# Kernel tuning notes

Measured on AMD Instinct MI355X. Metric: run time of the kernel, lower is better.

Reference implementation:

```python
import jax, jax.numpy as jnp
import numpy as np

V, E, H = 32000, 512, 1024
B, T = 16, 256
EPS = 1e-5

def setup_inputs() -> dict:
    key = jax.random.key(0)
    ks = jax.random.split(key, 20)
    s = lambda *shape: 0.02
    inp = {
        'input': jax.random.randint(ks[0], (B, T), 0, V),
        'embd': jax.random.normal(ks[1], (V, E), jnp.float32) * 0.02,
        # layer 0 GRUCell (input E -> H)
        'Wih0': jax.random.normal(ks[2], (3 * H, E), jnp.float32) * 0.02,
        'Whh0': jax.random.normal(ks[3], (3 * H, H), jnp.float32) * 0.02,
        'bih0': jnp.zeros((3 * H,), jnp.float32),
        'bhh0': jnp.zeros((3 * H,), jnp.float32),
        'ln0_w': jnp.ones((H,), jnp.float32),
        'ln0_b': jnp.zeros((H,), jnp.float32),
        # layer 1 GRUCell (H -> H)
        'Wih1': jax.random.normal(ks[4], (3 * H, H), jnp.float32) * 0.02,
        'Whh1': jax.random.normal(ks[5], (3 * H, H), jnp.float32) * 0.02,
        'bih1': jnp.zeros((3 * H,), jnp.float32),
        'bhh1': jnp.zeros((3 * H,), jnp.float32),
        'ln1_w': jnp.ones((H,), jnp.float32),
        'ln1_b': jnp.zeros((H,), jnp.float32),
        # head: Linear(H,H) -> LeakyReLU -> LayerNorm -> Linear(H,V)
        'W1': jax.random.normal(ks[6], (H, H), jnp.float32) * 0.02,
        'b1': jnp.zeros((H,), jnp.float32),
        'ln2_w': jnp.ones((H,), jnp.float32),
        'ln2_b': jnp.zeros((H,), jnp.float32),
        'W2': jax.random.normal(ks[7], (V, H), jnp.float32) * 0.02,
        'b2': jnp.zeros((V,), jnp.float32),
    }
    return inp

def _layernorm(x, w, b):
    m = jnp.mean(x, axis=-1, keepdims=True)
    v = jnp.var(x, axis=-1, keepdims=True)
    return (x - m) * jax.lax.rsqrt(v + EPS) * w + b

def _gru_cell(x, h, Wih, Whh, bih, bhh):
    gi = x @ Wih.T + bih  # [B, 3H]
    gh = h @ Whh.T + bhh
    ir, iz, inn = jnp.split(gi, 3, axis=-1)
    hr, hz, hn = jnp.split(gh, 3, axis=-1)
    r = jax.nn.sigmoid(ir + hr)
    z = jax.nn.sigmoid(iz + hz)
    n = jnp.tanh(inn + r * hn)
    return (1.0 - z) * n + z * h

def reference(input, embd, Wih0, Whh0, bih0, bhh0, ln0_w, ln0_b,
              Wih1, Whh1, bih1, bhh1, ln1_w, ln1_b,
              W1, b1, ln2_w, ln2_b, W2, b2):
    x = embd[input]                      # [B, T, E]
    xT = jnp.swapaxes(x, 0, 1)           # [T, B, E]
    Bn = input.shape[0]
    h0 = jnp.zeros((Bn, H), x.dtype)
    h1 = jnp.zeros((Bn, H), x.dtype)

    def step(carry, xt):
        h0, h1 = carry
        h0 = _layernorm(_gru_cell(xt, h0, Wih0, Whh0, bih0, bhh0), ln0_w, ln0_b)
        h1 = _layernorm(_gru_cell(h0, h1, Wih1, Whh1, bih1, bhh1), ln1_w, ln1_b)
        a = jax.nn.leaky_relu(h1 @ W1.T + b1, negative_slope=0.01)
        a = _layernorm(a, ln2_w, ln2_b)
        logits = a @ W2.T + b2           # [B, V]
        return (h0, h1), logits

    _, outs = jax.lax.scan(step, (h0, h1), xT)   # [T, B, V]
    return jnp.swapaxes(outs, 0, 1)              # [B, T, V]
```

## Files before the change

kernel.cpp:

```cpp
#include <hip/hip_runtime.h>
#include <stdint.h>
#include <math.h>

#define TT 256
#define VOCAB 32000
#define LN_EPS 1e-5
#define NBLK 256

typedef __attribute__((ext_vector_type(8))) short bf16x8;
typedef __attribute__((ext_vector_type(4))) float f32x4;

__device__ __forceinline__ float bf2f(short s) {
  return __uint_as_float(((uint32_t)(uint16_t)s) << 16);
}
__device__ __forceinline__ short f2bf(float f) {
  uint32_t u = __float_as_uint(f);
  u += 0x7fffu + ((u >> 16) & 1u);
  return (short)(u >> 16);
}
__device__ __forceinline__ f32x4 mfma16(bf16x8 a, bf16x8 b, f32x4 c) {
  return __builtin_amdgcn_mfma_f32_16x16x32_bf16(a, b, c, 0, 0, 0);
}

__device__ __forceinline__ double cload(const double* p) {
  return __hip_atomic_load(p, __ATOMIC_RELAXED, __HIP_MEMORY_SCOPE_AGENT);
}
__device__ __forceinline__ void cstore(double* p, double v) {
  __hip_atomic_store(p, v, __ATOMIC_RELAXED, __HIP_MEMORY_SCOPE_AGENT);
}

__global__ void k_gi0(const int* __restrict__ input, const float* __restrict__ embd,
                      const float* __restrict__ Wih0, const float* __restrict__ bih0,
                      double* __restrict__ gi0) {
  const int t = blockIdx.x >> 4;
  const int cg = blockIdx.x & 15;
  const int tid = threadIdx.x;
  __shared__ float xs[16][512];
  for (int idx = tid; idx < 16 * 512; idx += 256) {
    const int r = idx >> 9, j = idx & 511;
    const int tok = input[r * TT + t];
    xs[r][j] = embd[(size_t)tok * 512 + j];
  }
  __syncthreads();
  const int row = tid >> 4, ct = tid & 15;
  for (int i = 0; i < 12; ++i) {
    const int c = cg * 192 + ct + 16 * i;
    const float4* wp = (const float4*)(Wih0 + (size_t)c * 512);
    const float4* xp = (const float4*)&xs[row][0];
    double acc = 0.0;
#pragma unroll 8
    for (int j4 = 0; j4 < 128; ++j4) {
      const float4 w = wp[j4];
      const float4 x = xp[j4];
      acc = fma((double)x.x, (double)w.x, acc);
      acc = fma((double)x.y, (double)w.y, acc);
      acc = fma((double)x.z, (double)w.z, acc);
      acc = fma((double)x.w, (double)w.w, acc);
    }
    gi0[((size_t)t * 16 + row) * 3072 + c] = acc + (double)bih0[c];
  }
}

struct SP {
  const float *Whh0, *bhh0, *ln0w, *ln0b;
  const float *Wih1, *Whh1, *bih1, *bhh1, *ln1w, *ln1b;
  const double* gi0;
  double *h0ring, *h1ring;
  float* h1hist;
  int* bar;
};

__device__ __forceinline__ void stageC(const double* __restrict__ hrow,
                                       const float* __restrict__ lnw,
                                       const float* __restrict__ lnb,
                                       const int l, double* __restrict__ a,
                                       double& m_out, double& rs_out) {
  double s = 0.0, q = 0.0;
#pragma unroll
  for (int jj = 0; jj < 8; ++jj) {
    const double x0 = cload(hrow + jj * 128 + l * 2);
    const double x1 = cload(hrow + jj * 128 + l * 2 + 1);
    a[jj*2] = x0; a[jj*2+1] = x1;
    s += x0 + x1; q += x0*x0 + x1*x1;
  }
#pragma unroll
  for (int mk = 1; mk <= 32; mk <<= 1) { s += __shfl_xor(s, mk); q += __shfl_xor(q, mk); }
  const double m = s * (1.0 / 1024.0);
  const double rs = 1.0 / sqrt(q * (1.0 / 1024.0) - m * m + LN_EPS);
#pragma unroll
  for (int jj = 0; jj < 8; ++jj) {
    const float2 lw = *(const float2*)(lnw + jj * 128 + l * 2);
    const float2 lb = *(const float2*)(lnb + jj * 128 + l * 2);
    a[jj*2]   = (a[jj*2]   - m) * rs * (double)lw.x + (double)lb.x;
    a[jj*2+1] = (a[jj*2+1] - m) * rs * (double)lw.y + (double)lb.y;
  }
  m_out = m; rs_out = rs;
}

__launch_bounds__(512, 1)
__global__ void k_recur(SP A) {
  __shared__ float wlds[36][1024];
  __shared__ double sPre[36][16];
  __shared__ double sM0[16], sR0[16], sM1[16], sR1[16];
  const int tid = threadIdx.x;
  const int w = tid >> 6;
  const int l = tid & 63;
  const int bid = blockIdx.x;
  const int col0 = bid * 4;

  for (int idx = tid; idx < 36 * 1024; idx += 512) {
    const int j = idx >> 10, k = idx & 1023;
    const int jj = (j < 12) ? j : (j < 24 ? j - 12 : j - 24);
    const int g = jj % 3, ci = jj / 3;
    const float* W = (j < 12) ? A.Whh0 : (j < 24 ? A.Wih1 : A.Whh1);
    wlds[j][k] = W[(size_t)(g * 1024 + col0 + ci) * 1024 + k];
  }
  __syncthreads();

  for (int p = 0; p <= TT; ++p) {
    const bool doL0 = (p < TT);
    const int t1 = p - 1;
    double ar0[16], ar1[16];

    if (p >= 1) {
      const double* base = A.h0ring + (size_t)((p - 1) & 1) * 16384;
      double ma, ra, mb, rb;
      stageC(base + (2 * w) * 1024, A.ln0w, A.ln0b, l, ar0, ma, ra);
      stageC(base + (2 * w + 1) * 1024, A.ln0w, A.ln0b, l, ar1, mb, rb);
      if (l == 0) { sM0[2*w] = ma; sR0[2*w] = ra; sM0[2*w+1] = mb; sR0[2*w+1] = rb; }
      const int j0 = doL0 ? 0 : 12;
      for (int j = j0; j < 24; ++j) {
        double c0 = 0.0, c1 = 0.0;
#pragma unroll
        for (int jj = 0; jj < 8; ++jj) {
          const float2 wv = *(const float2*)&wlds[j][jj * 128 + l * 2];
          const double wx = (double)wv.x, wy = (double)wv.y;
          c0 = fma(wx, ar0[jj*2], c0); c0 = fma(wy, ar0[jj*2+1], c0);
          c1 = fma(wx, ar1[jj*2], c1); c1 = fma(wy, ar1[jj*2+1], c1);
        }
#pragma unroll
        for (int mk = 1; mk <= 32; mk <<= 1) { c0 += __shfl_xor(c0, mk); c1 += __shfl_xor(c1, mk); }
        if (l == 0) { sPre[j][2*w] = c0; sPre[j][2*w+1] = c1; }
      }
      if (t1 > 0) {
        const double* base1 = A.h1ring + (size_t)((t1 - 1) & 1) * 16384;
        stageC(base1 + (2 * w) * 1024, A.ln1w, A.ln1b, l, ar0, ma, ra);
        stageC(base1 + (2 * w + 1) * 1024, A.ln1w, A.ln1b, l, ar1, mb, rb);
        if (l == 0) { sM1[2*w] = ma; sR1[2*w] = ra; sM1[2*w+1] = mb; sR1[2*w+1] = rb; }
        for (int j = 24; j < 36; ++j) {
          double c0 = 0.0, c1 = 0.0;
#pragma unroll
          for (int jj = 0; jj < 8; ++jj) {
            const float2 wv = *(const float2*)&wlds[j][jj * 128 + l * 2];
            const double wx = (double)wv.x, wy = (double)wv.y;
            c0 = fma(wx, ar0[jj*2], c0); c0 = fma(wy, ar0[jj*2+1], c0);
            c1 = fma(wx, ar1[jj*2], c1); c1 = fma(wy, ar1[jj*2+1], c1);
          }
#pragma unroll
          for (int mk = 1; mk <= 32; mk <<= 1) { c0 += __shfl_xor(c0, mk); c1 += __shfl_xor(c1, mk); }
          if (l == 0) { sPre[j][2*w] = c0; sPre[j][2*w+1] = c1; }
        }
      }
    }
    __syncthreads();

    if (doL0 && tid < 64) {
      const int r = tid >> 2, ci = tid & 3;
      const int c = col0 + ci;
      const int t0 = p;
      double ghr, ghz, ghn, hprev;
      if (t0 > 0) {
        ghr = sPre[ci*3+0][r] + (double)A.bhh0[c];
        ghz = sPre[ci*3+1][r] + (double)A.bhh0[c + 1024];
        ghn = sPre[ci*3+2][r] + (double)A.bhh0[c + 2048];
        const double praw = cload(A.h0ring + (size_t)((t0 - 1) & 1) * 16384 + r * 1024 + c);
        hprev = (praw - sM0[r]) * sR0[r] * (double)A.ln0w[c] + (double)A.ln0b[c];
      } else {
        ghr = (double)A.bhh0[c]; ghz = (double)A.bhh0[c + 1024]; ghn = (double)A.bhh0[c + 2048];
        hprev = 0.0;
      }
      const double* gp = A.gi0 + ((size_t)t0 * 16 + r) * 3072 + c;
      const double gir = gp[0], giz = gp[1024], gin = gp[2048];
      const double rg = 1.0 / (1.0 + exp(-(gir + ghr)));
      const double zg = 1.0 / (1.0 + exp(-(giz + ghz)));
      const double ng = tanh(gin + rg * ghn);
      cstore(A.h0ring + (size_t)(t0 & 1) * 16384 + r * 1024 + c, (1.0 - zg) * ng + zg * hprev);
    }
    if (t1 >= 0 && tid >= 64 && tid < 128) {
      const int r = (tid - 64) >> 2, ci = (tid - 64) & 3;
      const int c = col0 + ci;
      const double gir = sPre[12+ci*3+0][r] + (double)A.bih1[c];
      const double giz = sPre[12+ci*3+1][r] + (double)A.bih1[c + 1024];
      const double gin = sPre[12+ci*3+2][r] + (double)A.bih1[c + 2048];
      double ghr, ghz, ghn, hprev;
      if (t1 > 0) {
        ghr = sPre[24+ci*3+0][r] + (double)A.bhh1[c];
        ghz = sPre[24+ci*3+1][r] + (double)A.bhh1[c + 1024];
        ghn = sPre[24+ci*3+2][r] + (double)A.bhh1[c + 2048];
        const double praw = cload(A.h1ring + (size_t)((t1 - 1) & 1) * 16384 + r * 1024 + c);
        hprev = (praw - sM1[r]) * sR1[r] * (double)A.ln1w[c] + (double)A.ln1b[c];
      } else {
        ghr = (double)A.bhh1[c]; ghz = (double)A.bhh1[c + 1024]; ghn = (double)A.bhh1[c + 2048];
        hprev = 0.0;
      }
      const double rg = 1.0 / (1.0 + exp(-(gir + ghr)));
      const double zg = 1.0 / (1.0 + exp(-(giz + ghz)));
      const double ng = tanh(gin + rg * ghn);
      const double hnew = (1.0 - zg) * ng + zg * hprev;
      cstore(A.h1ring + (size_t)(t1 & 1) * 16384 + r * 1024 + c, hnew);
      A.h1hist[((size_t)t1 * 16 + r) * 1024 + c] = (float)hnew;
    }

    __syncthreads();
    if (tid == 0) {
      __hip_atomic_fetch_add(A.bar, 1, __ATOMIC_RELAXED, __HIP_MEMORY_SCOPE_AGENT);
      const int target = NBLK * (p + 1);
      while (__hip_atomic_load(A.bar, __ATOMIC_RELAXED, __HIP_MEMORY_SCOPE_AGENT) < target) {
        __builtin_amdgcn_s_sleep(2);
      }
    }
    __syncthreads();
  }
}

__launch_bounds__(512, 2)
__global__ void k_headpre(const float* __restrict__ h1hist, const float* __restrict__ ln1w,
                          const float* __restrict__ ln1b, const float* __restrict__ W1,
                          const float* __restrict__ b1, short* __restrict__ araw) {
  const int tid = threadIdx.x;
  const int row = tid >> 5, ks = tid & 31;
  const size_t m = (size_t)blockIdx.x * 16 + row;
  const float* hp = h1hist + m * 1024;
  float a[32];
  float s = 0.f, q = 0.f;
#pragma unroll
  for (int g = 0; g < 8; ++g) {
    const float4 v = *(const float4*)(hp + g * 128 + ks * 4);
    a[g*4+0] = v.x; a[g*4+1] = v.y; a[g*4+2] = v.z; a[g*4+3] = v.w;
    s += v.x + v.y + v.z + v.w;
    q += v.x * v.x + v.y * v.y + v.z * v.z + v.w * v.w;
  }
#pragma unroll
  for (int mk = 1; mk <= 16; mk <<= 1) { s += __shfl_xor(s, mk); q += __shfl_xor(q, mk); }
  const float mn = s * (1.f / 1024.f);
  const float rs = rsqrtf(q * (1.f / 1024.f) - mn * mn + 1e-5f);
#pragma unroll
  for (int g = 0; g < 8; ++g) {
    const float4 lw = *(const float4*)(ln1w + g * 128 + ks * 4);
    const float4 lb = *(const float4*)(ln1b + g * 128 + ks * 4);
    a[g*4+0] = (a[g*4+0] - mn) * rs * lw.x + lb.x;
    a[g*4+1] = (a[g*4+1] - mn) * rs * lw.y + lb.y;
    a[g*4+2] = (a[g*4+2] - mn) * rs * lw.z + lb.z;
    a[g*4+3] = (a[g*4+3] - mn) * rs * lw.w + lb.w;
  }
  for (int c = 0; c < 1024; ++c) {
    const float4* wp = (const float4*)(W1 + (size_t)c * 1024);
    float acc = 0.f;
#pragma unroll
    for (int g = 0; g < 8; ++g) {
      const float4 w = wp[g * 32 + ks];
      acc = fmaf(a[g*4+0], w.x, acc); acc = fmaf(a[g*4+1], w.y, acc);
      acc = fmaf(a[g*4+2], w.z, acc); acc = fmaf(a[g*4+3], w.w, acc);
    }
#pragma unroll
    for (int mk = 1; mk <= 16; mk <<= 1) acc += __shfl_xor(acc, mk);
    if (ks == 0) {
      const float y = acc + b1[c];
      araw[m * 1024 + c] = f2bf(y > 0.f ? y : 0.01f * y);
    }
  }
}

__global__ void k_head(const short* __restrict__ araw, const float* __restrict__ W2,
                       const float* __restrict__ ln2w, const float* __restrict__ ln2b,
                       const float* __restrict__ b2, float* __restrict__ C) {
  __shared__ __align__(16) short As[128 * 64];
  __shared__ __align__(16) short Bs[128 * 64];
  __shared__ float rowm[128], rowr[128];
  __shared__ float lnw_s[1024], lnb_s[1024];
  __shared__ float ps[256], pq[256];
  const int tid = threadIdx.x;
  const long brow = (long)blockIdx.y * 128;
  const long bcol = (long)blockIdx.x * 128;

  for (int i = tid; i < 1024; i += 256) { lnw_s[i] = ln2w[i]; lnb_s[i] = ln2b[i]; }
  {
    const int r2 = tid >> 1, hf = tid & 1;
    const short* ap = araw + (brow + r2) * 1024 + hf * 512;
    float s = 0.f, q = 0.f;
    for (int j = 0; j < 512; j += 8) {
      const bf16x8 v = *(const bf16x8*)(ap + j);
#pragma unroll
      for (int e = 0; e < 8; ++e) { const float x = bf2f(v[e]); s += x; q += x * x; }
    }
    ps[tid] = s; pq[tid] = q;
  }
  __syncthreads();
  if (tid < 128) {
    const float s = ps[2 * tid] + ps[2 * tid + 1];
    const float q = pq[2 * tid] + pq[2 * tid + 1];
    const float m = s * (1.f / 1024.f);
    rowm[tid] = m;
    rowr[tid] = rsqrtf(q * (1.f / 1024.f) - m * m + 1e-5f);
  }
  __syncthreads();

  const int l = tid & 63;
  const int w = tid >> 6;
  const int wm = w >> 1, wn = w & 1;
  const int lane15 = l & 15, lgrp = l >> 4;
  f32x4 zero4 = {0.f, 0.f, 0.f, 0.f};
  f32x4 acc[4][4];
#pragma unroll
  for (int ri = 0; ri < 4; ++ri)
#pragma unroll
    for (int ci = 0; ci < 4; ++ci) acc[ri][ci] = zero4;

  for (int k0 = 0; k0 < 1024; k0 += 64) {
    __syncthreads();
#pragma unroll
    for (int i = 0; i < 4; ++i) {
      const int c = tid + i * 256;
      const int r = c >> 3, cc = c & 7;
      const int k = k0 + cc * 8;
      {
        const bf16x8 v = *(const bf16x8*)(araw + (brow + r) * 1024 + k);
        const float mm = rowm[r], rr = rowr[r];
        bf16x8 o;
#pragma unroll
        for (int e = 0; e < 8; ++e)
          o[e] = f2bf((bf2f(v[e]) - mm) * rr * lnw_s[k + e] + lnb_s[k + e]);
        *(bf16x8*)&As[r * 64 + cc * 8] = o;
      }
      {
        const float4* bp = (const float4*)(W2 + (bcol + r) * 1024 + k);
        const float4 v0 = bp[0], v1 = bp[1];
        bf16x8 o;
        o[0] = f2bf(v0.x); o[1] = f2bf(v0.y); o[2] = f2bf(v0.z); o[3] = f2bf(v0.w);
        o[4] = f2bf(v1.x); o[5] = f2bf(v1.y); o[6] = f2bf(v1.z); o[7] = f2bf(v1.w);
        *(bf16x8*)&Bs[r * 64 + cc * 8] = o;
      }
    }
    __syncthreads();
#pragma unroll
    for (int kk = 0; kk < 2; ++kk) {
      const int ko = kk * 32 + lgrp * 8;
      bf16x8 av[4], bv[4];
#pragma unroll
      for (int ri = 0; ri < 4; ++ri) av[ri] = *(const bf16x8*)&As[(wm * 64 + ri * 16 + lane15) * 64 + ko];
#pragma unroll
      for (int ci = 0; ci < 4; ++ci) bv[ci] = *(const bf16x8*)&Bs[(wn * 64 + ci * 16 + lane15) * 64 + ko];
#pragma unroll
      for (int ri = 0; ri < 4; ++ri)
#pragma unroll
        for (int ci = 0; ci < 4; ++ci) acc[ri][ci] = mfma16(av[ri], bv[ci], acc[ri][ci]);
    }
  }
#pragma unroll
  for (int ri = 0; ri < 4; ++ri)
#pragma unroll
    for (int ci = 0; ci < 4; ++ci)
#pragma unroll
      for (int i = 0; i < 4; ++i) {
        const long mrow = brow + wm * 64 + ri * 16 + lgrp * 4 + i;
        const long ncol = bcol + wn * 64 + ci * 16 + lane15;
        const int tq = (int)(mrow >> 4), b = (int)(mrow & 15);
        C[(size_t)b * TT * VOCAB + (size_t)tq * VOCAB + ncol] = acc[ri][ci][i] + b2[ncol];
      }
}

extern "C" void kernel_launch(void* const* d_in, const int* in_sizes, int n_in,
                              void* d_out, int out_size, void* d_ws, size_t ws_size,
                              hipStream_t stream) {
  const int* input = (const int*)d_in[0];
  const float* embd = (const float*)d_in[1];
  const float* Wih0 = (const float*)d_in[2];
  const float* Whh0 = (const float*)d_in[3];
  const float* bih0 = (const float*)d_in[4];
  const float* bhh0 = (const float*)d_in[5];
  const float* ln0w = (const float*)d_in[6];
  const float* ln0b = (const float*)d_in[7];
  const float* Wih1 = (const float*)d_in[8];
  const float* Whh1 = (const float*)d_in[9];
  const float* bih1 = (const float*)d_in[10];
  const float* bhh1 = (const float*)d_in[11];
  const float* ln1w = (const float*)d_in[12];
  const float* ln1b = (const float*)d_in[13];
  const float* W1 = (const float*)d_in[14];
  const float* b1 = (const float*)d_in[15];
  const float* ln2w = (const float*)d_in[16];
  const float* ln2b = (const float*)d_in[17];
  const float* W2 = (const float*)d_in[18];
  const float* b2 = (const float*)d_in[19];
  float* out = (float*)d_out;

  char* ws = (char*)d_ws;
  size_t off = 0;
  auto alloc = [&](size_t bytes) -> char* {
    char* p = ws + off;
    off = (off + bytes + 255) & ~(size_t)255;
    return p;
  };
  double* h0ring = (double*)alloc(2ull * 16 * 1024 * 8);
  double* h1ring = (double*)alloc(2ull * 16 * 1024 * 8);
  float* h1hist = (float*)alloc(4096ull * 1024 * 4);
  short* araw = (short*)alloc(4096ull * 1024 * 2);
  int* bar = (int*)alloc(256);

  hipMemsetAsync(bar, 0, 256, stream);

  double* gi0 = (double*)d_out;

  k_gi0<<<4096, 256, 0, stream>>>(input, embd, Wih0, bih0, gi0);

  SP A;
  A.Whh0 = Whh0; A.bhh0 = bhh0; A.ln0w = ln0w; A.ln0b = ln0b;
  A.Wih1 = Wih1; A.Whh1 = Whh1; A.bih1 = bih1; A.bhh1 = bhh1;
  A.ln1w = ln1w; A.ln1b = ln1b;
  A.gi0 = gi0; A.h0ring = h0ring; A.h1ring = h1ring; A.h1hist = h1hist;
  A.bar = bar;
  k_recur<<<NBLK, 512, 0, stream>>>(A);

  k_headpre<<<256, 512, 0, stream>>>(h1hist, ln1w, ln1b, W1, b1, araw);

  k_head<<<dim3(250, 32), 256, 0, stream>>>(araw, W2, ln2w, ln2b, b2, out);
}
```

Before: 15.99 ms.

## Hierarchical grid barrier, early ring loads, and pre-converted bf16 W2 for head

The grid barrier in the recurrent kernel becomes two-level: blocks first count within groups of eight, and only one leader per group touches the global counter and then releases its group through a per-group flag. This is meant to cut atomic contention on a single address at every timestep. Both layers' hidden-state rows are now loaded from the rings together before the layer-norm stats and dot products, so the load latencies can overlap. W2 is converted to bf16 once by a separate kernel, so the head GEMM reads half the bytes and skips per-tile conversion, at the cost of an extra pass over W2 and more workspace; the old path is kept if the workspace is too small.

```diff
diff --git a/kernel.cpp b/kernel.cpp
--- a/kernel.cpp
+++ b/kernel.cpp
@@ -70,17 +70,23 @@
   int* bar;
 };
 
-__device__ __forceinline__ void stageC(const double* __restrict__ hrow,
-                                       const float* __restrict__ lnw,
-                                       const float* __restrict__ lnb,
-                                       const int l, double* __restrict__ a,
-                                       double& m_out, double& rs_out) {
+__device__ __forceinline__ void loadR(const double* __restrict__ hrow, const int l,
+                                      double* __restrict__ a) {
+#pragma unroll
+  for (int jj = 0; jj < 8; ++jj) {
+    a[jj*2]   = cload(hrow + jj * 128 + l * 2);
+    a[jj*2+1] = cload(hrow + jj * 128 + l * 2 + 1);
+  }
+}
+
+__device__ __forceinline__ void statsLN(double* __restrict__ a,
+                                        const float* __restrict__ lnw,
+                                        const float* __restrict__ lnb,
+                                        const int l, double& m_out, double& rs_out) {
   double s = 0.0, q = 0.0;
 #pragma unroll
   for (int jj = 0; jj < 8; ++jj) {
-    const double x0 = cload(hrow + jj * 128 + l * 2);
-    const double x1 = cload(hrow + jj * 128 + l * 2 + 1);
-    a[jj*2] = x0; a[jj*2+1] = x1;
+    const double x0 = a[jj*2], x1 = a[jj*2+1];
     s += x0 + x1; q += x0*x0 + x1*x1;
   }
 #pragma unroll
@@ -120,13 +126,20 @@
   for (int p = 0; p <= TT; ++p) {
     const bool doL0 = (p < TT);
     const int t1 = p - 1;
-    double ar0[16], ar1[16];
+    double a0a[16], a0b[16], a1a[16], a1b[16];
 
     if (p >= 1) {
-      const double* base = A.h0ring + (size_t)((p - 1) & 1) * 16384;
+      const double* base0 = A.h0ring + (size_t)((p - 1) & 1) * 16384;
+      loadR(base0 + (2 * w) * 1024, l, a0a);
+      loadR(base0 + (2 * w + 1) * 1024, l, a0b);
+      if (t1 > 0) {
+        const double* base1 = A.h1ring + (size_t)((t1 - 1) & 1) * 16384;
+        loadR(base1 + (2 * w) * 1024, l, a1a);
+        loadR(base1 + (2 * w + 1) * 1024, l, a1b);
+      }
       double ma, ra, mb, rb;
-      stageC(base + (2 * w) * 1024, A.ln0w, A.ln0b, l, ar0, ma, ra);
-      stageC(base + (2 * w + 1) * 1024, A.ln0w, A.ln0b, l, ar1, mb, rb);
+      statsLN(a0a, A.ln0w, A.ln0b, l, ma, ra);
+      statsLN(a0b, A.ln0w, A.ln0b, l, mb, rb);
       if (l == 0) { sM0[2*w] = ma; sR0[2*w] = ra; sM0[2*w+1] = mb; sR0[2*w+1] = rb; }
       const int j0 = doL0 ? 0 : 12;
       for (int j = j0; j < 24; ++j) {
@@ -135,17 +148,16 @@
         for (int jj = 0; jj < 8; ++jj) {
           const float2 wv = *(const float2*)&wlds[j][jj * 128 + l * 2];
           const double wx = (double)wv.x, wy = (double)wv.y;
-          c0 = fma(wx, ar0[jj*2], c0); c0 = fma(wy, ar0[jj*2+1], c0);
-          c1 = fma(wx, ar1[jj*2], c1); c1 = fma(wy, ar1[jj*2+1], c1);
+          c0 = fma(wx, a0a[jj*2], c0); c0 = fma(wy, a0a[jj*2+1], c0);
+          c1 = fma(wx, a0b[jj*2], c1); c1 = fma(wy, a0b[jj*2+1], c1);
         }
 #pragma unroll
         for (int mk = 1; mk <= 32; mk <<= 1) { c0 += __shfl_xor(c0, mk); c1 += __shfl_xor(c1, mk); }
         if (l == 0) { sPre[j][2*w] = c0; sPre[j][2*w+1] = c1; }
       }
       if (t1 > 0) {
-        const double* base1 = A.h1ring + (size_t)((t1 - 1) & 1) * 16384;
-        stageC(base1 + (2 * w) * 1024, A.ln1w, A.ln1b, l, ar0, ma, ra);
-        stageC(base1 + (2 * w + 1) * 1024, A.ln1w, A.ln1b, l, ar1, mb, rb);
+        statsLN(a1a, A.ln1w, A.ln1b, l, ma, ra);
+        statsLN(a1b, A.ln1w, A.ln1b, l, mb, rb);
         if (l == 0) { sM1[2*w] = ma; sR1[2*w] = ra; sM1[2*w+1] = mb; sR1[2*w+1] = rb; }
         for (int j = 24; j < 36; ++j) {
           double c0 = 0.0, c1 = 0.0;
@@ -153,8 +165,8 @@
           for (int jj = 0; jj < 8; ++jj) {
             const float2 wv = *(const float2*)&wlds[j][jj * 128 + l * 2];
             const double wx = (double)wv.x, wy = (double)wv.y;
-            c0 = fma(wx, ar0[jj*2], c0); c0 = fma(wy, ar0[jj*2+1], c0);
-            c1 = fma(wx, ar1[jj*2], c1); c1 = fma(wy, ar1[jj*2+1], c1);
+            c0 = fma(wx, a1a[jj*2], c0); c0 = fma(wy, a1a[jj*2+1], c0);
+            c1 = fma(wx, a1b[jj*2], c1); c1 = fma(wy, a1b[jj*2+1], c1);
           }
 #pragma unroll
           for (int mk = 1; mk <= 32; mk <<= 1) { c0 += __shfl_xor(c0, mk); c1 += __shfl_xor(c1, mk); }
@@ -213,10 +225,21 @@
 
     __syncthreads();
     if (tid == 0) {
-      __hip_atomic_fetch_add(A.bar, 1, __ATOMIC_RELAXED, __HIP_MEMORY_SCOPE_AGENT);
-      const int target = NBLK * (p + 1);
-      while (__hip_atomic_load(A.bar, __ATOMIC_RELAXED, __HIP_MEMORY_SCOPE_AGENT) < target) {
-        __builtin_amdgcn_s_sleep(2);
+      const int g = bid >> 3;
+      int* grpC = A.bar + g * 32;
+      int* glob = A.bar + 32 * 32;
+      int* rel  = A.bar + 33 * 32 + g * 32;
+      const int my = __hip_atomic_fetch_add(grpC, 1, __ATOMIC_RELAXED, __HIP_MEMORY_SCOPE_AGENT);
+      if (my == 8 * (p + 1) - 1) {
+        __hip_atomic_fetch_add(glob, 1, __ATOMIC_RELAXED, __HIP_MEMORY_SCOPE_AGENT);
+        while (__hip_atomic_load(glob, __ATOMIC_RELAXED, __HIP_MEMORY_SCOPE_AGENT) < 32 * (p + 1)) {
+          __builtin_amdgcn_s_sleep(2);
+        }
+        __hip_atomic_store(rel, p + 1, __ATOMIC_RELAXED, __HIP_MEMORY_SCOPE_AGENT);
+      } else {
+        while (__hip_atomic_load(rel, __ATOMIC_RELAXED, __HIP_MEMORY_SCOPE_AGENT) < p + 1) {
+          __builtin_amdgcn_s_sleep(8);
+        }
       }
     }
     __syncthreads();
@@ -271,7 +294,14 @@
   }
 }
 
-__global__ void k_head(const short* __restrict__ araw, const float* __restrict__ W2,
+__global__ void k_w2q(const float* __restrict__ W2, short* __restrict__ W2q) {
+  const int n = 32000 * 1024;
+  for (int i = blockIdx.x * blockDim.x + threadIdx.x; i < n; i += gridDim.x * blockDim.x)
+    W2q[i] = f2bf(W2[i]);
+}
+
+template <int BW2>
+__global__ void k_head(const short* __restrict__ araw, const void* __restrict__ Bsrc,
                        const float* __restrict__ ln2w, const float* __restrict__ ln2b,
                        const float* __restrict__ b2, float* __restrict__ C) {
   __shared__ __align__(16) short As[128 * 64];
@@ -332,8 +362,12 @@
           o[e] = f2bf((bf2f(v[e]) - mm) * rr * lnw_s[k + e] + lnb_s[k + e]);
         *(bf16x8*)&As[r * 64 + cc * 8] = o;
       }
-      {
-        const float4* bp = (const float4*)(W2 + (bcol + r) * 1024 + k);
+      if (BW2) {
+        const short* bq = (const short*)Bsrc;
+        *(bf16x8*)&Bs[r * 64 + cc * 8] = *(const bf16x8*)&bq[(bcol + r) * 1024 + k];
+      } else {
+        const float* bw = (const float*)Bsrc;
+        const float4* bp = (const float4*)(bw + (bcol + r) * 1024 + k);
         const float4 v0 = bp[0], v1 = bp[1];
         bf16x8 o;
         o[0] = f2bf(v0.x); o[1] = f2bf(v0.y); o[2] = f2bf(v0.z); o[3] = f2bf(v0.w);
@@ -405,9 +439,13 @@
   double* h1ring = (double*)alloc(2ull * 16 * 1024 * 8);
   float* h1hist = (float*)alloc(4096ull * 1024 * 4);
   short* araw = (short*)alloc(4096ull * 1024 * 2);
-  int* bar = (int*)alloc(256);
-
-  hipMemsetAsync(bar, 0, 256, stream);
+  int* bar = (int*)alloc(16384);
+  const size_t base_need = off;
+  short* W2q = (short*)alloc(32000ull * 1024 * 2);
+  const bool useW2q = (ws_size >= off);
+  (void)base_need;
+
+  hipMemsetAsync(bar, 0, 16384, stream);
 
   double* gi0 = (double*)d_out;
 
@@ -423,5 +461,10 @@
 
   k_headpre<<<256, 512, 0, stream>>>(h1hist, ln1w, ln1b, W1, b1, araw);
 
-  k_head<<<dim3(250, 32), 256, 0, stream>>>(araw, W2, ln2w, ln2b, b2, out);
-}
+  if (useW2q) {
+    k_w2q<<<2048, 256, 0, stream>>>(W2, W2q);
+    k_head<1><<<dim3(250, 32), 256, 0, stream>>>(araw, W2q, ln2w, ln2b, b2, out);
+  } else {
+    k_head<0><<<dim3(250, 32), 256, 0, stream>>>(araw, W2, ln2w, ln2b, b2, out);
+  }
+}
```

Result: faster. 15.40 ms (-3.7%).
